# Optimization experiments

Measured on AMD Instinct MI355X. Metric: run time of the kernel, lower is better.

## Reference

```python
import jax, jax.numpy as jnp
import numpy as np

MARGIN = 1.0

def _pairwise_sqdist(z):
    # ||zi - zj||^2 = ||zi||^2 + ||zj||^2 - 2 zi.zj
    sq = jnp.sum(z * z, axis=-1)  # [N]
    d2 = sq[:, None] + sq[None, :] - 2.0 * (z @ z.T)
    return jnp.maximum(d2, 0.0)

def _safe_sqrt(d2):
    # sqrt with well-defined gradient at 0 (matches cdist values; diag = 0)
    pos = d2 > 0.0
    return jnp.where(pos, jnp.sqrt(jnp.where(pos, d2, 1.0)), 0.0)

def setup_inputs() -> dict:
    key = jax.random.key(0)
    k1, k2 = jax.random.split(key)
    z = jax.random.normal(k1, (8192, 128), dtype=jnp.float32)
    labels = jax.random.randint(k2, (8192,), 0, 100, dtype=jnp.int64)
    return {"z": z, "labels": labels}

def reference(z, labels):
    d2 = _pairwise_sqdist(z)              # [N, N] squared distances
    dist = _safe_sqrt(d2)                 # [N, N] distances
    label_eq = labels[:, None] == labels[None, :]
    pos = jnp.where(label_eq, d2, 0.0)
    neg = jnp.where(label_eq, 0.0, jnp.square(jax.nn.relu(MARGIN - dist)))
    return jnp.mean(pos + neg)
```

## Files before the change

### kernel.cpp

```cpp
#include <hip/hip_runtime.h>
#include <stdint.h>


#define NROWS 8192
#define DIMK  128
#define NB    64
#define NPERS 512

typedef __attribute__((ext_vector_type(4))) float f32x4;

#define AS_GLOBAL __attribute__((address_space(1)))
#define AS_LDS    __attribute__((address_space(3)))

__global__ __launch_bounds__(256) void prep_kernel(
    const float* __restrict__ z, unsigned char* __restrict__ zb,
    float* __restrict__ sq) {
  int tid = threadIdx.x;
  int row = (blockIdx.x << 3) + (tid >> 5);
  int c32 = tid & 31;
  float4 x = ((const float4*)(z + (size_t)row * DIMK))[c32];
  int u = __builtin_amdgcn_cvt_pk_fp8_f32(x.x, x.y, 0, false);
  u     = __builtin_amdgcn_cvt_pk_fp8_f32(x.z, x.w, u, true);
  float r0 = __builtin_amdgcn_cvt_f32_fp8(u, 0);
  float r1 = __builtin_amdgcn_cvt_f32_fp8(u, 1);
  float r2 = __builtin_amdgcn_cvt_f32_fp8(u, 2);
  float r3 = __builtin_amdgcn_cvt_f32_fp8(u, 3);
  float s = (r0 * r0 + r1 * r1) + (r2 * r2 + r3 * r3);
  int k0 = c32 << 2;
  int g  = (((k0 >> 3) & 3) << 2) | (k0 >> 5);
  int p  = ((g ^ (row & 15)) << 3) + (k0 & 7);
  *(uint32_t*)(zb + (size_t)row * DIMK + p) = (uint32_t)u;
  #pragma unroll
  for (int off = 16; off; off >>= 1) s += __shfl_down(s, off, 32);
  if (c32 == 0) sq[row] = s;
}

__device__ __forceinline__ void decode_tile_x(int x, int n, int& bi, int& bj) {
  int rem = n, k = 0, len = NB - x;
  while (rem >= len) { rem -= len; ++k; len -= 8; }
  bi = x + (k << 3);
  bj = bi + rem;
}

__global__ __launch_bounds__(512, 4) void loss_kernel(
    const unsigned char* __restrict__ zb, const float* __restrict__ sq,
    const int* __restrict__ labels, float* __restrict__ out) {
  __shared__ __align__(16) unsigned char buf[2][32768];
  __shared__ float red[8];

  int tid = threadIdx.x, lane = tid & 63, wave = tid >> 6;
  int wm = wave >> 1, wn = wave & 1;
  int lc = lane & 15;
  int q  = lane >> 4;

  float psum_acc = 0.f;

  int x = blockIdx.x & 7;
  int s = blockIdx.x >> 3;
  int tcount = 288 - 8 * x;
  int n = s;

  int bi, bj;
  decode_tile_x(x, n, bi, bj);

  {
    const unsigned char* Ab = zb + (((size_t)bi << 7) * DIMK);
    const unsigned char* Bb = zb + (((size_t)bj << 7) * DIMK);
    #pragma unroll
    for (int it = 0; it < 2; ++it) {
      int L0 = (it << 9) + (wave << 6);
      __builtin_amdgcn_global_load_lds(
          (const AS_GLOBAL void*)(uintptr_t)(Ab + (size_t)(L0 + lane) * 16),
          (AS_LDS void*)(uintptr_t)(&buf[0][(size_t)L0 * 16]), 16, 0, 0);
      __builtin_amdgcn_global_load_lds(
          (const AS_GLOBAL void*)(uintptr_t)(Bb + (size_t)(L0 + lane) * 16),
          (AS_LDS void*)(uintptr_t)(&buf[0][16384 + (size_t)L0 * 16]), 16, 0, 0);
    }
  }

  int cur = 0;
  for (;; n += 64) {
    int nn = n + 64;
    bool hasNext = nn < tcount;

    asm volatile("s_waitcnt vmcnt(0)" ::: "memory");
    __syncthreads();

    int bin = bi, bjn = bj;
    if (hasNext) {
      decode_tile_x(x, nn, bin, bjn);
      int nc = cur ^ 1;
      const unsigned char* Ab = zb + (((size_t)bin << 7) * DIMK);
      const unsigned char* Bb = zb + (((size_t)bjn << 7) * DIMK);
      #pragma unroll
      for (int it = 0; it < 2; ++it) {
        int L0 = (it << 9) + (wave << 6);
        __builtin_amdgcn_global_load_lds(
            (const AS_GLOBAL void*)(uintptr_t)(Ab + (size_t)(L0 + lane) * 16),
            (AS_LDS void*)(uintptr_t)(&buf[nc][(size_t)L0 * 16]), 16, 0, 0);
        __builtin_amdgcn_global_load_lds(
            (const AS_GLOBAL void*)(uintptr_t)(Bb + (size_t)(L0 + lane) * 16),
            (AS_LDS void*)(uintptr_t)(&buf[nc][16384 + (size_t)L0 * 16]), 16, 0, 0);
      }
    }

    const unsigned char* ldsA = &buf[cur][0];
    const unsigned char* ldsB = &buf[cur][16384];

    f32x4 acc[2][4] = {};
    #pragma unroll
    for (int ks = 0; ks < 4; ++ks) {
      int so = ((((q << 2) | ks) ^ lc) << 3);
      long a0 = *(const long*)(ldsA + ((wm << 5)      + lc) * 128 + so);
      long a1 = *(const long*)(ldsA + ((wm << 5) + 16 + lc) * 128 + so);
      long b0 = *(const long*)(ldsB + ((wn << 6)      + lc) * 128 + so);
      long b1 = *(const long*)(ldsB + ((wn << 6) + 16 + lc) * 128 + so);
      long b2 = *(const long*)(ldsB + ((wn << 6) + 32 + lc) * 128 + so);
      long b3 = *(const long*)(ldsB + ((wn << 6) + 48 + lc) * 128 + so);
      acc[0][0] = __builtin_amdgcn_mfma_f32_16x16x32_fp8_fp8(a0, b0, acc[0][0], 0, 0, 0);
      acc[0][1] = __builtin_amdgcn_mfma_f32_16x16x32_fp8_fp8(a0, b1, acc[0][1], 0, 0, 0);
      acc[0][2] = __builtin_amdgcn_mfma_f32_16x16x32_fp8_fp8(a0, b2, acc[0][2], 0, 0, 0);
      acc[0][3] = __builtin_amdgcn_mfma_f32_16x16x32_fp8_fp8(a0, b3, acc[0][3], 0, 0, 0);
      acc[1][0] = __builtin_amdgcn_mfma_f32_16x16x32_fp8_fp8(a1, b0, acc[1][0], 0, 0, 0);
      acc[1][1] = __builtin_amdgcn_mfma_f32_16x16x32_fp8_fp8(a1, b1, acc[1][1], 0, 0, 0);
      acc[1][2] = __builtin_amdgcn_mfma_f32_16x16x32_fp8_fp8(a1, b2, acc[1][2], 0, 0, 0);
      acc[1][3] = __builtin_amdgcn_mfma_f32_16x16x32_fp8_fp8(a1, b3, acc[1][3], 0, 0, 0);
    }

    const float* sqA = sq     + ((size_t)bi << 7);
    const int*   laA = labels + ((size_t)bi << 7);
    const float* sqB = sq     + ((size_t)bj << 7);
    const int*   laB = labels + ((size_t)bj << 7);

    int r0 = q << 2;
    float sn_[4]; int ln_[4];
    #pragma unroll
    for (int j = 0; j < 4; ++j) {
      int nidx = (wn << 6) + (j << 4) + lc;
      sn_[j] = sqB[nidx]; ln_[j] = laB[nidx];
    }
    float ps0 = 0.f, ps1 = 0.f, ps2 = 0.f, ps3 = 0.f;
    float mnall = 1e30f;
    #pragma unroll
    for (int i = 0; i < 2; ++i) {
      int mb = (wm << 5) + (i << 4) + r0;
      f32x4 sm4 = *(const f32x4*)&sqA[mb];
      int4  lm4 = *(const int4*)&laA[mb];
      #pragma unroll
      for (int j = 0; j < 4; ++j) {
        float d0  = fmaf(-2.f, acc[i][j][0], sm4[0] + sn_[j]);
        float d1  = fmaf(-2.f, acc[i][j][1], sm4[1] + sn_[j]);
        float d2_ = fmaf(-2.f, acc[i][j][2], sm4[2] + sn_[j]);
        float d3  = fmaf(-2.f, acc[i][j][3], sm4[3] + sn_[j]);
        mnall = fminf(mnall, fminf(fminf(d0, d1), fminf(d2_, d3)));
        ps0 += (lm4.x == ln_[j]) ? d0  : 0.f;
        ps1 += (lm4.y == ln_[j]) ? d1  : 0.f;
        ps2 += (lm4.z == ln_[j]) ? d2_ : 0.f;
        ps3 += (lm4.w == ln_[j]) ? d3  : 0.f;
      }
    }
    if (__builtin_expect(__any(mnall < 1.f), 0)) {
      ps0 = ps1 = ps2 = ps3 = 0.f;
      #pragma unroll
      for (int i = 0; i < 2; ++i) {
        int mb = (wm << 5) + (i << 4) + r0;
        f32x4 sm4 = *(const f32x4*)&sqA[mb];
        int4  lm4 = *(const int4*)&laA[mb];
        #pragma unroll
        for (int j = 0; j < 4; ++j) {
          float dc, tt;
          dc = fmaxf(fmaf(-2.f, acc[i][j][0], sm4[0] + sn_[j]), 0.f);
          tt = fmaxf(1.f - sqrtf(dc), 0.f);
          ps0 += (lm4.x == ln_[j]) ? dc : tt * tt;
          dc = fmaxf(fmaf(-2.f, acc[i][j][1], sm4[1] + sn_[j]), 0.f);
          tt = fmaxf(1.f - sqrtf(dc), 0.f);
          ps1 += (lm4.y == ln_[j]) ? dc : tt * tt;
          dc = fmaxf(fmaf(-2.f, acc[i][j][2], sm4[2] + sn_[j]), 0.f);
          tt = fmaxf(1.f - sqrtf(dc), 0.f);
          ps2 += (lm4.z == ln_[j]) ? dc : tt * tt;
          dc = fmaxf(fmaf(-2.f, acc[i][j][3], sm4[3] + sn_[j]), 0.f);
          tt = fmaxf(1.f - sqrtf(dc), 0.f);
          ps3 += (lm4.w == ln_[j]) ? dc : tt * tt;
        }
      }
    }
    float w = (bi == bj) ? 1.f : 2.f;
    psum_acc += w * ((ps0 + ps1) + (ps2 + ps3));

    if (!hasNext) break;
    bi = bin; bj = bjn; cur ^= 1;
  }

  psum_acc *= (1.f / (8192.f * 8192.f));
  #pragma unroll
  for (int off = 32; off; off >>= 1) psum_acc += __shfl_down(psum_acc, off);
  if (lane == 0) red[wave] = psum_acc;
  __syncthreads();
  if (tid == 0) {
    float sum = 0.f;
    #pragma unroll
    for (int k = 0; k < 8; ++k) sum += red[k];
    atomicAdd(out, sum);
  }
}

extern "C" void kernel_launch(void* const* d_in, const int* in_sizes, int n_in,
                              void* d_out, int out_size, void* d_ws, size_t ws_size,
                              hipStream_t stream) {
  const float* z      = (const float*)d_in[0];
  const int*   labels = (const int*)d_in[1];
  float*       out    = (float*)d_out;
  unsigned char* zb   = (unsigned char*)d_ws;
  float* sq           = (float*)((char*)d_ws + (size_t)NROWS * DIMK);

  prep_kernel<<<NROWS / 8, 256, 0, stream>>>(z, zb, sq);
  loss_kernel<<<NPERS, 512, 0, stream>>>(zb, sq, labels, out);
}
```

Baseline: 73.98 us.

## Load fp32 tiles directly in loss kernel and convert to fp8 in-register

The prep kernel no longer writes a pre-swizzled fp8 copy of z. The loss kernel now reads fp32 rows from global memory, converts them to fp8 in registers, and writes them into a single LDS buffer with the same swizzle. The double-buffered async global-to-LDS loads are replaced by register prefetch of the next A tile during compute, plus extra barriers around the LDS writes. This removes a global round-trip and halves LDS, but reads four times more bytes per tile and serializes the B-tile load after compute.

```diff
diff --git a/kernel.cpp b/kernel.cpp
--- a/kernel.cpp
+++ b/kernel.cpp
@@ -9,12 +9,8 @@
 
 typedef __attribute__((ext_vector_type(4))) float f32x4;
 
-#define AS_GLOBAL __attribute__((address_space(1)))
-#define AS_LDS    __attribute__((address_space(3)))
-
 __global__ __launch_bounds__(256) void prep_kernel(
-    const float* __restrict__ z, unsigned char* __restrict__ zb,
-    float* __restrict__ sq) {
+    const float* __restrict__ z, float* __restrict__ sq) {
   int tid = threadIdx.x;
   int row = (blockIdx.x << 3) + (tid >> 5);
   int c32 = tid & 31;
@@ -26,10 +22,6 @@
   float r2 = __builtin_amdgcn_cvt_f32_fp8(u, 2);
   float r3 = __builtin_amdgcn_cvt_f32_fp8(u, 3);
   float s = (r0 * r0 + r1 * r1) + (r2 * r2 + r3 * r3);
-  int k0 = c32 << 2;
-  int g  = (((k0 >> 3) & 3) << 2) | (k0 >> 5);
-  int p  = ((g ^ (row & 15)) << 3) + (k0 & 7);
-  *(uint32_t*)(zb + (size_t)row * DIMK + p) = (uint32_t)u;
   #pragma unroll
   for (int off = 16; off; off >>= 1) s += __shfl_down(s, off, 32);
   if (c32 == 0) sq[row] = s;
@@ -42,10 +34,30 @@
   bj = bi + rem;
 }
 
+#define CVT8(xs, dw) do {                                                    \
+  _Pragma("unroll")                                                          \
+  for (int i = 0; i < 8; ++i) {                                              \
+    int u_ = __builtin_amdgcn_cvt_pk_fp8_f32((xs)[i].x, (xs)[i].y, 0, false);\
+    u_     = __builtin_amdgcn_cvt_pk_fp8_f32((xs)[i].z, (xs)[i].w, u_, true);\
+    (dw)[i] = (uint32_t)u_;                                                  \
+  }                                                                          \
+} while (0)
+
+#define WRITE8(dw, base) do {                                                \
+  _Pragma("unroll")                                                          \
+  for (int i = 0; i < 8; ++i) {                                              \
+    int f_ = (i << 9) + tid;                                                 \
+    int r_ = f_ >> 5, c_ = f_ & 31, k0_ = c_ << 2;                           \
+    int g_ = (((k0_ >> 3) & 3) << 2) | (k0_ >> 5);                           \
+    *(uint32_t*)(&lds_all[(base) + r_ * 128 +                                \
+                          ((g_ ^ (r_ & 15)) << 3) + (k0_ & 7)]) = (dw)[i];   \
+  }                                                                          \
+} while (0)
+
 __global__ __launch_bounds__(512, 4) void loss_kernel(
-    const unsigned char* __restrict__ zb, const float* __restrict__ sq,
+    const float* __restrict__ z, const float* __restrict__ sq,
     const int* __restrict__ labels, float* __restrict__ out) {
-  __shared__ __align__(16) unsigned char buf[2][32768];
+  __shared__ __align__(16) unsigned char lds_all[32768];
   __shared__ float red[8];
 
   int tid = threadIdx.x, lane = tid & 63, wave = tid >> 6;
@@ -58,54 +70,39 @@
   int x = blockIdx.x & 7;
   int s = blockIdx.x >> 3;
   int tcount = 288 - 8 * x;
-  int n = s;
 
   int bi, bj;
-  decode_tile_x(x, n, bi, bj);
+  decode_tile_x(x, s, bi, bj);
 
   {
-    const unsigned char* Ab = zb + (((size_t)bi << 7) * DIMK);
-    const unsigned char* Bb = zb + (((size_t)bj << 7) * DIMK);
-    #pragma unroll
-    for (int it = 0; it < 2; ++it) {
-      int L0 = (it << 9) + (wave << 6);
-      __builtin_amdgcn_global_load_lds(
-          (const AS_GLOBAL void*)(uintptr_t)(Ab + (size_t)(L0 + lane) * 16),
-          (AS_LDS void*)(uintptr_t)(&buf[0][(size_t)L0 * 16]), 16, 0, 0);
-      __builtin_amdgcn_global_load_lds(
-          (const AS_GLOBAL void*)(uintptr_t)(Bb + (size_t)(L0 + lane) * 16),
-          (AS_LDS void*)(uintptr_t)(&buf[0][16384 + (size_t)L0 * 16]), 16, 0, 0);
-    }
+    const float4* Za = (const float4*)z + ((size_t)bi << 12);
+    const float4* Zb = (const float4*)z + ((size_t)bj << 12);
+    float4 xsA[8], xsB[8];
+    #pragma unroll
+    for (int i = 0; i < 8; ++i) xsA[i] = Za[(i << 9) + tid];
+    #pragma unroll
+    for (int i = 0; i < 8; ++i) xsB[i] = Zb[(i << 9) + tid];
+    uint32_t dwA[8], dwB[8];
+    CVT8(xsA, dwA); WRITE8(dwA, 0);
+    CVT8(xsB, dwB); WRITE8(dwB, 16384);
+    __syncthreads();
   }
 
-  int cur = 0;
-  for (;; n += 64) {
+  for (int n = s;;) {
     int nn = n + 64;
     bool hasNext = nn < tcount;
 
-    asm volatile("s_waitcnt vmcnt(0)" ::: "memory");
-    __syncthreads();
-
     int bin = bi, bjn = bj;
+    float4 xsA[8];
     if (hasNext) {
       decode_tile_x(x, nn, bin, bjn);
-      int nc = cur ^ 1;
-      const unsigned char* Ab = zb + (((size_t)bin << 7) * DIMK);
-      const unsigned char* Bb = zb + (((size_t)bjn << 7) * DIMK);
-      #pragma unroll
-      for (int it = 0; it < 2; ++it) {
-        int L0 = (it << 9) + (wave << 6);
-        __builtin_amdgcn_global_load_lds(
-            (const AS_GLOBAL void*)(uintptr_t)(Ab + (size_t)(L0 + lane) * 16),
-            (AS_LDS void*)(uintptr_t)(&buf[nc][(size_t)L0 * 16]), 16, 0, 0);
-        __builtin_amdgcn_global_load_lds(
-            (const AS_GLOBAL void*)(uintptr_t)(Bb + (size_t)(L0 + lane) * 16),
-            (AS_LDS void*)(uintptr_t)(&buf[nc][16384 + (size_t)L0 * 16]), 16, 0, 0);
-      }
-    }
-
-    const unsigned char* ldsA = &buf[cur][0];
-    const unsigned char* ldsB = &buf[cur][16384];
+      const float4* Za = (const float4*)z + ((size_t)bin << 12);
+      #pragma unroll
+      for (int i = 0; i < 8; ++i) xsA[i] = Za[(i << 9) + tid];
+    }
+
+    const unsigned char* ldsA = &lds_all[0];
+    const unsigned char* ldsB = &lds_all[16384];
 
     f32x4 acc[2][4] = {};
     #pragma unroll
@@ -188,7 +185,23 @@
     psum_acc += w * ((ps0 + ps1) + (ps2 + ps3));
 
     if (!hasNext) break;
-    bi = bin; bj = bjn; cur ^= 1;
+
+    uint32_t dwA[8];
+    CVT8(xsA, dwA);
+    float4 xsB[8];
+    {
+      const float4* Zb = (const float4*)z + ((size_t)bjn << 12);
+      #pragma unroll
+      for (int i = 0; i < 8; ++i) xsB[i] = Zb[(i << 9) + tid];
+    }
+    __syncthreads();
+    WRITE8(dwA, 0);
+    uint32_t dwB[8];
+    CVT8(xsB, dwB);
+    WRITE8(dwB, 16384);
+    __syncthreads();
+
+    bi = bin; bj = bjn; n = nn;
   }
 
   psum_acc *= (1.f / (8192.f * 8192.f));
@@ -210,9 +223,8 @@
   const float* z      = (const float*)d_in[0];
   const int*   labels = (const int*)d_in[1];
   float*       out    = (float*)d_out;
-  unsigned char* zb   = (unsigned char*)d_ws;
-  float* sq           = (float*)((char*)d_ws + (size_t)NROWS * DIMK);
-
-  prep_kernel<<<NROWS / 8, 256, 0, stream>>>(z, zb, sq);
-  loss_kernel<<<NPERS, 512, 0, stream>>>(zb, sq, labels, out);
-}
+  float*       sq     = (float*)d_ws;
+
+  prep_kernel<<<NROWS / 8, 256, 0, stream>>>(z, sq);
+  loss_kernel<<<NPERS, 512, 0, stream>>>(z, sq, labels, out);
+}
```

After: 81.66 us. 10.4% more time.
